# Optimization experiments

Measured on AMD Instinct MI355X. Metric: run time of the kernel, lower is better.

Reference implementation:

```python
import jax, jax.numpy as jnp
import numpy as np

BS = 32768
NIN = 512
E = 8          # num_experts
T = 2          # num_tasks
H = 256        # num_neurons_expert
NT = 1         # num_neurons_tower


def setup_inputs() -> dict:
    key = jax.random.key(0)
    ks = jax.random.split(key, 7)
    s_in = 1.0 / np.sqrt(NIN)
    s_h = 1.0 / np.sqrt(H)
    return {
        "xv": jax.random.normal(ks[0], (BS, NIN), dtype=jnp.float32),
        "We": jax.random.uniform(ks[1], (E, NIN, H), dtype=jnp.float32, minval=-s_in, maxval=s_in),
        "be": jax.random.uniform(ks[2], (E, H), dtype=jnp.float32, minval=-s_in, maxval=s_in),
        "Wg": jax.random.uniform(ks[3], (T, NIN, E), dtype=jnp.float32, minval=-s_in, maxval=s_in),
        "bg": jax.random.uniform(ks[4], (T, E), dtype=jnp.float32, minval=-s_in, maxval=s_in),
        "Wt": jax.random.uniform(ks[5], (T, H, NT), dtype=jnp.float32, minval=-s_h, maxval=s_h),
        "bt": jax.random.uniform(ks[6], (T, NT), dtype=jnp.float32, minval=-s_h, maxval=s_h),
        "bs": BS,
    }


def reference(xv, We, be, Wg, bg, Wt, bt, bs):
    # Experts: [bs, E, H] (dropout is identity in eval mode)
    out_experts = jax.nn.relu(jnp.einsum("bi,eih->beh", xv, We) + be[None, :, :])
    # Gates: [bs, T, E], softmax over experts
    gates = jax.nn.softmax(jnp.einsum("bi,tie->bte", xv, Wg) + bg[None, :, :], axis=-1)
    # Gated combine: [bs, T, H]
    input_towers = jnp.einsum("bte,beh->bth", gates, out_experts)
    # Towers: [bs, T, NT] -> squeeze NT=1 -> [bs, T]
    out_towers = jax.nn.relu(jnp.einsum("bth,thn->btn", input_towers, Wt) + bt[None, :, :])
    out = jax.nn.sigmoid(out_towers[:, :, 0])  # [bs, T]
    return (out[:, 0], out[:, 1])
```

## Files before the change

### kernel.cpp

```cpp
#include <hip/hip_runtime.h>

typedef __attribute__((ext_vector_type(8))) short short8;
typedef __attribute__((ext_vector_type(4))) float floatx4;
typedef __attribute__((ext_vector_type(4))) float f32x4;

#define BS   32768

__device__ __forceinline__ unsigned short f2bf(float f) {
  unsigned int u = __float_as_uint(f);
  u += 0x7fffu + ((u >> 16) & 1u);
  return (unsigned short)(u >> 16);
}

__global__ void prep_weT(const float* __restrict__ We, unsigned short* __restrict__ WeT) {
  int e  = blockIdx.x >> 6;
  int kc = blockIdx.x & 63;
  int h  = threadIdx.x;
  short8 pk;
#pragma unroll
  for (int j = 0; j < 8; ++j)
    pk[j] = (short)f2bf(We[e * 131072 + (kc * 8 + j) * 256 + h]);
  *reinterpret_cast<short8*>(&WeT[e * 131072 + h * 512 + kc * 8]) = pk;
}

__global__ void prep_wgT(const float* __restrict__ Wg, unsigned short* __restrict__ WgT) {
  int row = blockIdx.x;
  int t = row >> 3, e = row & 7;
  int lane = threadIdx.x;
  short8 pk;
#pragma unroll
  for (int j = 0; j < 8; ++j)
    pk[j] = (short)f2bf(Wg[t * 4096 + (lane * 8 + j) * 8 + e]);
  *reinterpret_cast<short8*>(&WgT[row * 512 + lane * 8]) = pk;
}

#define GLOAD16(SRC, DST) \
  __builtin_amdgcn_global_load_lds( \
      (const __attribute__((address_space(1))) unsigned int*)(SRC), \
      (__attribute__((address_space(3))) unsigned int*)(DST), 16, 0, 0)

__global__ __launch_bounds__(256) void conv_gates(
    const float* __restrict__ xv, const unsigned short* __restrict__ WgT,
    const float* __restrict__ bg, unsigned short* __restrict__ Abf,
    float* __restrict__ gates_ws)
{
  __shared__ __attribute__((aligned(16))) unsigned char bufA[65536];
  const int tid = threadIdx.x;
  const int b0  = blockIdx.x * 64;
  const int r8 = tid >> 3, kslot = tid & 7;
  const int mt = b0 >> 8;
  const int rc_base = b0 & 255;
  unsigned char* AbfB = reinterpret_cast<unsigned char*>(Abf);

#pragma unroll
  for (int pass = 0; pass < 2; ++pass) {
    int r = pass * 32 + r8;
    int r_c = rc_base + r;
    const float* xrow = xv + (size_t)(b0 + r) * 512;
    unsigned swz = (unsigned)((r & 7) << 4);
#pragma unroll
    for (int j = 0; j < 8; ++j) {
      int o = j * 8 + kslot;
      f32x4 v0 = *reinterpret_cast<const f32x4*>(xrow + o * 8);
      f32x4 v1 = *reinterpret_cast<const f32x4*>(xrow + o * 8 + 4);
      short8 pk;
      pk[0] = (short)f2bf(v0[0]); pk[1] = (short)f2bf(v0[1]);
      pk[2] = (short)f2bf(v0[2]); pk[3] = (short)f2bf(v0[3]);
      pk[4] = (short)f2bf(v1[0]); pk[5] = (short)f2bf(v1[1]);
      pk[6] = (short)f2bf(v1[2]); pk[7] = (short)f2bf(v1[3]);
      unsigned lb = ((unsigned)r << 10) + (((unsigned)(o * 16)) ^ swz);
      *reinterpret_cast<short8*>(&bufA[lb]) = pk;
      unsigned gb = (unsigned)((mt * 8 + j) * 32768) + (unsigned)(r_c * 128)
                  + (((unsigned)(kslot * 16)) ^ swz);
      *reinterpret_cast<short8*>(&AbfB[gb]) = pk;
    }
  }
  __syncthreads();

  const int wave = tid >> 6, lane = tid & 63;
  const int row16 = lane & 15, kgrp = lane >> 4;
  floatx4 gacc = {0.f, 0.f, 0.f, 0.f};
  const unsigned abase = ((unsigned)row16 << 10) + ((unsigned)kgrp << 4) + ((unsigned)wave << 14);
  const unsigned a_swz = (unsigned)((row16 & 7) << 4);
  const unsigned short* wg_lane = WgT + row16 * 512 + kgrp * 8;
#pragma unroll
  for (int ks = 0; ks < 16; ++ks) {
    short8 af = *reinterpret_cast<const short8*>(&bufA[(abase + (unsigned)(ks << 6)) ^ a_swz]);
    short8 bf = *reinterpret_cast<const short8*>(wg_lane + ks * 32);
    gacc = __builtin_amdgcn_mfma_f32_16x16x32_bf16(af, bf, gacc, 0, 0, 0);
  }
  float bgv = bg[row16];
#pragma unroll
  for (int j = 0; j < 4; ++j) {
    float v = gacc[j] + bgv;
    float mx = v;
    mx = fmaxf(mx, __shfl_xor(mx, 1));
    mx = fmaxf(mx, __shfl_xor(mx, 2));
    mx = fmaxf(mx, __shfl_xor(mx, 4));
    float p = __expf(v - mx);
    float s = p;
    s += __shfl_xor(s, 1);
    s += __shfl_xor(s, 2);
    s += __shfl_xor(s, 4);
    gates_ws[row16 * BS + b0 + wave * 16 + kgrp * 4 + j] = p / s;
  }
}

__global__ __launch_bounds__(512, 2) void mmoe_main(
    const unsigned short* __restrict__ Abf,
    const unsigned short* __restrict__ WeT,
    const float* __restrict__ gates_ws,
    const float* __restrict__ be,
    const float* __restrict__ Wt,
    float* __restrict__ acc_ws)
{
  __shared__ __attribute__((aligned(16))) unsigned char smem[131072];
  __shared__ float red_lds[4][256][2];

  const int tid = threadIdx.x, wave = tid >> 6, lane = tid & 63;
  const int row16 = lane & 15, kgrp = lane >> 4;
  const int wm = wave >> 2, wn = wave & 3;
  const int bid = blockIdx.x, e = bid & 7, mt = bid >> 3;

  const unsigned short* Asrc = Abf + (size_t)mt * 131072;
  const unsigned short* Bsrc = WeT + e * 131072;

  unsigned soffB[4];
#pragma unroll
  for (int i = 0; i < 4; ++i) {
    unsigned x = (unsigned)(i * 8192 + tid * 16);
    unsigned r = x >> 7;
    unsigned y = (x & 127u) ^ ((r & 7u) << 4);
    soffB[i] = r * 512u + (y >> 1);
  }
  const unsigned soffA0 = (unsigned)(tid * 8);

  unsigned char* Ab0 = smem;
  unsigned char* Ab1 = smem + 32768;
  unsigned char* Bb0 = smem + 65536;
  unsigned char* Bb1 = smem + 98304;

#pragma unroll
  for (int i = 0; i < 4; ++i)
    GLOAD16(Asrc + (i * 4096 + soffA0), Ab0 + (i * 8 + wave) * 1024);
#pragma unroll
  for (int i = 0; i < 4; ++i)
    GLOAD16(Bsrc + soffB[i], Bb0 + (i * 8 + wave) * 1024);

  floatx4 acc[8][4];
#pragma unroll
  for (int mf = 0; mf < 8; ++mf)
#pragma unroll
    for (int n = 0; n < 4; ++n) acc[mf][n] = (floatx4){0.f, 0.f, 0.f, 0.f};

  const unsigned swz = (unsigned)((row16 & 7) << 4);
  const unsigned bcol = (unsigned)(wn * 64 + row16);
  const unsigned arow = (unsigned)(wm * 128 + row16);

  for (int kc = 0; kc < 8; ++kc) {
    const int cur = kc & 1;
    if (kc < 7) {
      unsigned char* an = cur ? Ab0 : Ab1;
      unsigned char* bn = cur ? Bb0 : Bb1;
      const unsigned short* abase2 = Asrc + (kc + 1) * 16384;
      const unsigned short* bbase2 = Bsrc + (kc + 1) * 64;
#pragma unroll
      for (int i = 0; i < 4; ++i)
        GLOAD16(abase2 + (i * 4096 + soffA0), an + (i * 8 + wave) * 1024);
#pragma unroll
      for (int i = 0; i < 4; ++i)
        GLOAD16(bbase2 + soffB[i], bn + (i * 8 + wave) * 1024);
      asm volatile("s_waitcnt vmcnt(8)" ::: "memory");
    } else {
      asm volatile("s_waitcnt vmcnt(0)" ::: "memory");
    }
    __builtin_amdgcn_s_barrier();
    __builtin_amdgcn_sched_barrier(0);

    const unsigned char* ab = cur ? Ab1 : Ab0;
    const unsigned char* bb = cur ? Bb1 : Bb0;
    __builtin_amdgcn_s_setprio(1);
    short8 bf[2][4];
#pragma unroll
    for (int ks = 0; ks < 2; ++ks)
#pragma unroll
      for (int n = 0; n < 4; ++n)
        bf[ks][n] = *reinterpret_cast<const short8*>(
            &bb[(bcol + (unsigned)(n * 16)) * 128 + (((unsigned)(ks * 64 + kgrp * 16)) ^ swz)]);
#pragma unroll
    for (int mf = 0; mf < 8; ++mf) {
      const unsigned rb = (arow + (unsigned)(mf * 16)) * 128;
      short8 a0 = *reinterpret_cast<const short8*>(&ab[rb + (((unsigned)(kgrp * 16)) ^ swz)]);
      short8 a1 = *reinterpret_cast<const short8*>(&ab[rb + (((unsigned)(64 + kgrp * 16)) ^ swz)]);
#pragma unroll
      for (int n = 0; n < 4; ++n)
        acc[mf][n] = __builtin_amdgcn_mfma_f32_16x16x32_bf16(a0, bf[0][n], acc[mf][n], 0, 0, 0);
#pragma unroll
      for (int n = 0; n < 4; ++n)
        acc[mf][n] = __builtin_amdgcn_mfma_f32_16x16x32_bf16(a1, bf[1][n], acc[mf][n], 0, 0, 0);
    }
    __builtin_amdgcn_s_setprio(0);
    __builtin_amdgcn_s_barrier();
  }

  float bev[4], wtv[2][4];
#pragma unroll
  for (int n = 0; n < 4; ++n) bev[n] = be[e * 256 + wn * 64 + n * 16 + row16];
#pragma unroll
  for (int t = 0; t < 2; ++t)
#pragma unroll
    for (int n = 0; n < 4; ++n) wtv[t][n] = Wt[t * 256 + wn * 64 + n * 16 + row16];

#pragma unroll
  for (int mf = 0; mf < 8; ++mf) {
#pragma unroll
    for (int j = 0; j < 4; ++j) {
      float p0 = 0.f, p1 = 0.f;
#pragma unroll
      for (int n = 0; n < 4; ++n) {
        float r = fmaxf(acc[mf][n][j] + bev[n], 0.f);
        p0 = fmaf(r, wtv[0][n], p0);
        p1 = fmaf(r, wtv[1][n], p1);
      }
      p0 += __shfl_xor(p0, 1); p1 += __shfl_xor(p1, 1);
      p0 += __shfl_xor(p0, 2); p1 += __shfl_xor(p1, 2);
      p0 += __shfl_xor(p0, 4); p1 += __shfl_xor(p1, 4);
      p0 += __shfl_xor(p0, 8); p1 += __shfl_xor(p1, 8);
      if (row16 == 0) {
        int rw = wm * 128 + mf * 16 + kgrp * 4 + j;
        red_lds[wn][rw][0] = p0;
        red_lds[wn][rw][1] = p1;
      }
    }
  }
  __syncthreads();

  {
    int row = tid >> 1, t = tid & 1;
    float s = red_lds[0][row][t] + red_lds[1][row][t]
            + red_lds[2][row][t] + red_lds[3][row][t];
    float g = gates_ws[(t * 8 + e) * BS + mt * 256 + row];
    atomicAdd(&acc_ws[t * BS + mt * 256 + row], s * g);
  }
}

__global__ void finalize(const float* __restrict__ acc_ws, const float* __restrict__ bt,
                         float* __restrict__ out) {
  int i = blockIdx.x * 256 + threadIdx.x;
  int t = i >> 15;
  float s = fmaxf(acc_ws[i] + bt[t], 0.f);
  out[i] = 1.f / (1.f + __expf(-s));
}

extern "C" void kernel_launch(void* const* d_in, const int* in_sizes, int n_in,
                              void* d_out, int out_size, void* d_ws, size_t ws_size,
                              hipStream_t stream) {
  const float* xv = (const float*)d_in[0];
  const float* We = (const float*)d_in[1];
  const float* be = (const float*)d_in[2];
  const float* Wg = (const float*)d_in[3];
  const float* bg = (const float*)d_in[4];
  const float* Wt = (const float*)d_in[5];
  const float* bt = (const float*)d_in[6];
  float* out = (float*)d_out;

  unsigned char* ws = (unsigned char*)d_ws;
  unsigned short* WeT      = (unsigned short*)(ws);
  unsigned short* WgT      = (unsigned short*)(ws + (2u << 20));
  unsigned short* Abf      = (unsigned short*)(ws + (4u << 20));
  float*          gates_ws = (float*)(ws + (36u << 20));
  float*          acc_ws   = (float*)(ws + (38u << 20));

  hipMemsetAsync(acc_ws, 0, 2 * BS * sizeof(float), stream);
  prep_weT<<<512, 256, 0, stream>>>(We, WeT);
  prep_wgT<<<16, 64, 0, stream>>>(Wg, WgT);
  conv_gates<<<512, 256, 0, stream>>>(xv, WgT, bg, Abf, gates_ws);
  mmoe_main<<<1024, 512, 0, stream>>>(Abf, WeT, gates_ws, be, Wt, acc_ws);
  finalize<<<256, 256, 0, stream>>>(acc_ws, bt, out);
}
```

Before: 130.5 us.

## Split GEMM K-step into four phases interleaving prefetch with MFMA clusters

Restructures the double-buffered main loop into four phases per K tile. Each phase reads a pair of A fragments from LDS, issues part of the next tile's global-to-LDS loads, then runs a barrier-synchronised cluster of MFMAs at raised priority. The aim is to spread memory traffic across the compute and keep waves in lockstep, in the style of ping-pong scheduling. In exchange it adds many more barriers per iteration, and the prologue now waits for the whole first tile before starting.

```diff
diff --git a/kernel.cpp b/kernel.cpp
--- a/kernel.cpp
+++ b/kernel.cpp
@@ -146,6 +146,8 @@
 #pragma unroll
   for (int i = 0; i < 4; ++i)
     GLOAD16(Bsrc + soffB[i], Bb0 + (i * 8 + wave) * 1024);
+  asm volatile("s_waitcnt vmcnt(0)" ::: "memory");
+  __syncthreads();
 
   floatx4 acc[8][4];
 #pragma unroll
@@ -153,54 +155,134 @@
 #pragma unroll
     for (int n = 0; n < 4; ++n) acc[mf][n] = (floatx4){0.f, 0.f, 0.f, 0.f};
 
-  const unsigned swz = (unsigned)((row16 & 7) << 4);
+  const unsigned swz  = (unsigned)((row16 & 7) << 4);
   const unsigned bcol = (unsigned)(wn * 64 + row16);
   const unsigned arow = (unsigned)(wm * 128 + row16);
 
-  for (int kc = 0; kc < 8; ++kc) {
-    const int cur = kc & 1;
-    if (kc < 7) {
-      unsigned char* an = cur ? Ab0 : Ab1;
-      unsigned char* bn = cur ? Bb0 : Bb1;
-      const unsigned short* abase2 = Asrc + (kc + 1) * 16384;
-      const unsigned short* bbase2 = Bsrc + (kc + 1) * 64;
-#pragma unroll
-      for (int i = 0; i < 4; ++i)
-        GLOAD16(abase2 + (i * 4096 + soffA0), an + (i * 8 + wave) * 1024);
-#pragma unroll
-      for (int i = 0; i < 4; ++i)
-        GLOAD16(bbase2 + soffB[i], bn + (i * 8 + wave) * 1024);
-      asm volatile("s_waitcnt vmcnt(8)" ::: "memory");
-    } else {
-      asm volatile("s_waitcnt vmcnt(0)" ::: "memory");
-    }
-    __builtin_amdgcn_s_barrier();
+  for (int kt = 0; kt < 8; ++kt) {
     __builtin_amdgcn_sched_barrier(0);
-
+    const int cur = kt & 1;
     const unsigned char* ab = cur ? Ab1 : Ab0;
     const unsigned char* bb = cur ? Bb1 : Bb0;
-    __builtin_amdgcn_s_setprio(1);
+    unsigned char* an = cur ? Ab0 : Ab1;
+    unsigned char* bn = cur ? Bb0 : Bb1;
+    const unsigned short* aNext = Asrc + (kt + 1) * 16384;
+    const unsigned short* bNext = Bsrc + (kt + 1) * 64;
+
+    auto rdA = [&](int mf, int ks) -> short8 {
+      const unsigned rb = (arow + (unsigned)(mf * 16)) * 128;
+      return *reinterpret_cast<const short8*>(
+          &ab[rb + (((unsigned)(ks * 64 + kgrp * 16)) ^ swz)]);
+    };
+
     short8 bf[2][4];
-#pragma unroll
-    for (int ks = 0; ks < 2; ++ks)
-#pragma unroll
-      for (int n = 0; n < 4; ++n)
-        bf[ks][n] = *reinterpret_cast<const short8*>(
-            &bb[(bcol + (unsigned)(n * 16)) * 128 + (((unsigned)(ks * 64 + kgrp * 16)) ^ swz)]);
-#pragma unroll
-    for (int mf = 0; mf < 8; ++mf) {
-      const unsigned rb = (arow + (unsigned)(mf * 16)) * 128;
-      short8 a0 = *reinterpret_cast<const short8*>(&ab[rb + (((unsigned)(kgrp * 16)) ^ swz)]);
-      short8 a1 = *reinterpret_cast<const short8*>(&ab[rb + (((unsigned)(64 + kgrp * 16)) ^ swz)]);
-#pragma unroll
-      for (int n = 0; n < 4; ++n)
-        acc[mf][n] = __builtin_amdgcn_mfma_f32_16x16x32_bf16(a0, bf[0][n], acc[mf][n], 0, 0, 0);
-#pragma unroll
-      for (int n = 0; n < 4; ++n)
-        acc[mf][n] = __builtin_amdgcn_mfma_f32_16x16x32_bf16(a1, bf[1][n], acc[mf][n], 0, 0, 0);
-    }
-    __builtin_amdgcn_s_setprio(0);
-    __builtin_amdgcn_s_barrier();
+
+    {
+#pragma unroll
+      for (int ks = 0; ks < 2; ++ks)
+#pragma unroll
+        for (int n = 0; n < 4; ++n)
+          bf[ks][n] = *reinterpret_cast<const short8*>(
+              &bb[(bcol + (unsigned)(n * 16)) * 128 + (((unsigned)(ks * 64 + kgrp * 16)) ^ swz)]);
+      short8 p00 = rdA(0, 0), p01 = rdA(0, 1), p10 = rdA(1, 0), p11 = rdA(1, 1);
+      if (kt < 7) {
+#pragma unroll
+        for (int i = 0; i < 4; ++i)
+          GLOAD16(aNext + (i * 4096 + soffA0), an + (i * 8 + wave) * 1024);
+      }
+      asm volatile("s_waitcnt lgkmcnt(8)" ::: "memory");
+      __builtin_amdgcn_s_barrier();
+      asm volatile("s_waitcnt lgkmcnt(0)" ::: "memory");
+      __builtin_amdgcn_sched_barrier(0);
+      __builtin_amdgcn_s_setprio(1);
+#pragma unroll
+      for (int n = 0; n < 4; ++n)
+        acc[0][n] = __builtin_amdgcn_mfma_f32_16x16x32_bf16(p00, bf[0][n], acc[0][n], 0, 0, 0);
+#pragma unroll
+      for (int n = 0; n < 4; ++n)
+        acc[0][n] = __builtin_amdgcn_mfma_f32_16x16x32_bf16(p01, bf[1][n], acc[0][n], 0, 0, 0);
+#pragma unroll
+      for (int n = 0; n < 4; ++n)
+        acc[1][n] = __builtin_amdgcn_mfma_f32_16x16x32_bf16(p10, bf[0][n], acc[1][n], 0, 0, 0);
+#pragma unroll
+      for (int n = 0; n < 4; ++n)
+        acc[1][n] = __builtin_amdgcn_mfma_f32_16x16x32_bf16(p11, bf[1][n], acc[1][n], 0, 0, 0);
+      __builtin_amdgcn_s_setprio(0);
+      __builtin_amdgcn_s_barrier();
+    }
+
+    {
+      short8 p00 = rdA(2, 0), p01 = rdA(2, 1), p10 = rdA(3, 0), p11 = rdA(3, 1);
+      if (kt < 7) {
+#pragma unroll
+        for (int i = 0; i < 4; ++i)
+          GLOAD16(bNext + soffB[i], bn + (i * 8 + wave) * 1024);
+      }
+      __builtin_amdgcn_s_barrier();
+      asm volatile("s_waitcnt lgkmcnt(0)" ::: "memory");
+      __builtin_amdgcn_sched_barrier(0);
+      __builtin_amdgcn_s_setprio(1);
+#pragma unroll
+      for (int n = 0; n < 4; ++n)
+        acc[2][n] = __builtin_amdgcn_mfma_f32_16x16x32_bf16(p00, bf[0][n], acc[2][n], 0, 0, 0);
+#pragma unroll
+      for (int n = 0; n < 4; ++n)
+        acc[2][n] = __builtin_amdgcn_mfma_f32_16x16x32_bf16(p01, bf[1][n], acc[2][n], 0, 0, 0);
+#pragma unroll
+      for (int n = 0; n < 4; ++n)
+        acc[3][n] = __builtin_amdgcn_mfma_f32_16x16x32_bf16(p10, bf[0][n], acc[3][n], 0, 0, 0);
+#pragma unroll
+      for (int n = 0; n < 4; ++n)
+        acc[3][n] = __builtin_amdgcn_mfma_f32_16x16x32_bf16(p11, bf[1][n], acc[3][n], 0, 0, 0);
+      __builtin_amdgcn_s_setprio(0);
+      __builtin_amdgcn_s_barrier();
+    }
+
+    {
+      short8 p00 = rdA(4, 0), p01 = rdA(4, 1), p10 = rdA(5, 0), p11 = rdA(5, 1);
+      __builtin_amdgcn_s_barrier();
+      asm volatile("s_waitcnt lgkmcnt(0)" ::: "memory");
+      __builtin_amdgcn_sched_barrier(0);
+      __builtin_amdgcn_s_setprio(1);
+#pragma unroll
+      for (int n = 0; n < 4; ++n)
+        acc[4][n] = __builtin_amdgcn_mfma_f32_16x16x32_bf16(p00, bf[0][n], acc[4][n], 0, 0, 0);
+#pragma unroll
+      for (int n = 0; n < 4; ++n)
+        acc[4][n] = __builtin_amdgcn_mfma_f32_16x16x32_bf16(p01, bf[1][n], acc[4][n], 0, 0, 0);
+#pragma unroll
+      for (int n = 0; n < 4; ++n)
+        acc[5][n] = __builtin_amdgcn_mfma_f32_16x16x32_bf16(p10, bf[0][n], acc[5][n], 0, 0, 0);
+#pragma unroll
+      for (int n = 0; n < 4; ++n)
+        acc[5][n] = __builtin_amdgcn_mfma_f32_16x16x32_bf16(p11, bf[1][n], acc[5][n], 0, 0, 0);
+      __builtin_amdgcn_s_setprio(0);
+      __builtin_amdgcn_s_barrier();
+    }
+
+    {
+      short8 p00 = rdA(6, 0), p01 = rdA(6, 1), p10 = rdA(7, 0), p11 = rdA(7, 1);
+      if (kt < 7)
+        asm volatile("s_waitcnt vmcnt(0)" ::: "memory");
+      __builtin_amdgcn_s_barrier();
+      asm volatile("s_waitcnt lgkmcnt(0)" ::: "memory");
+      __builtin_amdgcn_sched_barrier(0);
+      __builtin_amdgcn_s_setprio(1);
+#pragma unroll
+      for (int n = 0; n < 4; ++n)
+        acc[6][n] = __builtin_amdgcn_mfma_f32_16x16x32_bf16(p00, bf[0][n], acc[6][n], 0, 0, 0);
+#pragma unroll
+      for (int n = 0; n < 4; ++n)
+        acc[6][n] = __builtin_amdgcn_mfma_f32_16x16x32_bf16(p01, bf[1][n], acc[6][n], 0, 0, 0);
+#pragma unroll
+      for (int n = 0; n < 4; ++n)
+        acc[7][n] = __builtin_amdgcn_mfma_f32_16x16x32_bf16(p10, bf[0][n], acc[7][n], 0, 0, 0);
+#pragma unroll
+      for (int n = 0; n < 4; ++n)
+        acc[7][n] = __builtin_amdgcn_mfma_f32_16x16x32_bf16(p11, bf[1][n], acc[7][n], 0, 0, 0);
+      __builtin_amdgcn_s_setprio(0);
+      __builtin_amdgcn_s_barrier();
+    }
   }
 
   float bev[4], wtv[2][4];
```

Result: faster. 124.9 us (-4.3%).

## Interleave LDS fragment reads with MFMA groups and stagger next-tile global loads

Applied to the files above, without the earlier changes.

The K-loop is fully unrolled, and the A-fragment LDS reads are split into four stages. Each stage's reads are issued before the previous stage's MFMA group, with lgkmcnt waits and sched_barriers, so LDS latency overlaps matrix math. The prefetch of the next tile is also split: A loads go out before the barrier and B loads go out mid-iteration, so the vmcnt wait only covers the older loads. This adds more registers for the in-flight fragments and relies on hand-placed counter waits, which could stall or raise register pressure if mistuned.

```diff
diff --git a/kernel.cpp b/kernel.cpp
--- a/kernel.cpp
+++ b/kernel.cpp
@@ -153,33 +153,39 @@
 #pragma unroll
     for (int n = 0; n < 4; ++n) acc[mf][n] = (floatx4){0.f, 0.f, 0.f, 0.f};
 
-  const unsigned swz = (unsigned)((row16 & 7) << 4);
+  const unsigned swz  = (unsigned)((row16 & 7) << 4);
   const unsigned bcol = (unsigned)(wn * 64 + row16);
   const unsigned arow = (unsigned)(wm * 128 + row16);
 
-  for (int kc = 0; kc < 8; ++kc) {
-    const int cur = kc & 1;
-    if (kc < 7) {
-      unsigned char* an = cur ? Ab0 : Ab1;
-      unsigned char* bn = cur ? Bb0 : Bb1;
-      const unsigned short* abase2 = Asrc + (kc + 1) * 16384;
-      const unsigned short* bbase2 = Bsrc + (kc + 1) * 64;
+#define RDA(AB, MF, KS) \
+  (*reinterpret_cast<const short8*>( \
+      &(AB)[(arow + (unsigned)((MF) * 16)) * 128 + (((unsigned)((KS) * 64 + kgrp * 16)) ^ swz)]))
+
+#define MFMA4(ACC, AV, BV) \
+  _Pragma("unroll") \
+  for (int n = 0; n < 4; ++n) \
+    ACC[n] = __builtin_amdgcn_mfma_f32_16x16x32_bf16(AV, BV[n], ACC[n], 0, 0, 0);
+
+#pragma unroll
+  for (int kt = 0; kt < 8; ++kt) {
+    const unsigned char* ab = (kt & 1) ? Ab1 : Ab0;
+    const unsigned char* bb = (kt & 1) ? Bb1 : Bb0;
+    unsigned char* an = (kt & 1) ? Ab0 : Ab1;
+    unsigned char* bn = (kt & 1) ? Bb0 : Bb1;
+    const unsigned short* aNext = Asrc + (kt + 1) * 16384;
+    const unsigned short* bNext = Bsrc + (kt + 1) * 64;
+
+    if (kt < 7) {
 #pragma unroll
       for (int i = 0; i < 4; ++i)
-        GLOAD16(abase2 + (i * 4096 + soffA0), an + (i * 8 + wave) * 1024);
-#pragma unroll
-      for (int i = 0; i < 4; ++i)
-        GLOAD16(bbase2 + soffB[i], bn + (i * 8 + wave) * 1024);
-      asm volatile("s_waitcnt vmcnt(8)" ::: "memory");
+        GLOAD16(aNext + (i * 4096 + soffA0), an + (i * 8 + wave) * 1024);
+      asm volatile("s_waitcnt vmcnt(4)" ::: "memory");
     } else {
       asm volatile("s_waitcnt vmcnt(0)" ::: "memory");
     }
     __builtin_amdgcn_s_barrier();
     __builtin_amdgcn_sched_barrier(0);
 
-    const unsigned char* ab = cur ? Ab1 : Ab0;
-    const unsigned char* bb = cur ? Bb1 : Bb0;
-    __builtin_amdgcn_s_setprio(1);
     short8 bf[2][4];
 #pragma unroll
     for (int ks = 0; ks < 2; ++ks)
@@ -187,21 +193,51 @@
       for (int n = 0; n < 4; ++n)
         bf[ks][n] = *reinterpret_cast<const short8*>(
             &bb[(bcol + (unsigned)(n * 16)) * 128 + (((unsigned)(ks * 64 + kgrp * 16)) ^ swz)]);
-#pragma unroll
-    for (int mf = 0; mf < 8; ++mf) {
-      const unsigned rb = (arow + (unsigned)(mf * 16)) * 128;
-      short8 a0 = *reinterpret_cast<const short8*>(&ab[rb + (((unsigned)(kgrp * 16)) ^ swz)]);
-      short8 a1 = *reinterpret_cast<const short8*>(&ab[rb + (((unsigned)(64 + kgrp * 16)) ^ swz)]);
-#pragma unroll
-      for (int n = 0; n < 4; ++n)
-        acc[mf][n] = __builtin_amdgcn_mfma_f32_16x16x32_bf16(a0, bf[0][n], acc[mf][n], 0, 0, 0);
-#pragma unroll
-      for (int n = 0; n < 4; ++n)
-        acc[mf][n] = __builtin_amdgcn_mfma_f32_16x16x32_bf16(a1, bf[1][n], acc[mf][n], 0, 0, 0);
+    short8 a00 = RDA(ab, 0, 0), a01 = RDA(ab, 0, 1);
+    short8 a10 = RDA(ab, 1, 0), a11 = RDA(ab, 1, 1);
+    short8 b00 = RDA(ab, 2, 0), b01 = RDA(ab, 2, 1);
+    short8 b10 = RDA(ab, 3, 0), b11 = RDA(ab, 3, 1);
+    asm volatile("s_waitcnt lgkmcnt(4)" ::: "memory");
+    __builtin_amdgcn_sched_barrier(0);
+    __builtin_amdgcn_s_setprio(1);
+    MFMA4(acc[0], a00, bf[0]); MFMA4(acc[0], a01, bf[1]);
+    MFMA4(acc[1], a10, bf[0]); MFMA4(acc[1], a11, bf[1]);
+    __builtin_amdgcn_s_setprio(0);
+
+    if (kt < 7) {
+#pragma unroll
+      for (int i = 0; i < 4; ++i)
+        GLOAD16(bNext + soffB[i], bn + (i * 8 + wave) * 1024);
     }
+    short8 c00 = RDA(ab, 4, 0), c01 = RDA(ab, 4, 1);
+    short8 c10 = RDA(ab, 5, 0), c11 = RDA(ab, 5, 1);
+    asm volatile("s_waitcnt lgkmcnt(4)" ::: "memory");
+    __builtin_amdgcn_sched_barrier(0);
+    __builtin_amdgcn_s_setprio(1);
+    MFMA4(acc[2], b00, bf[0]); MFMA4(acc[2], b01, bf[1]);
+    MFMA4(acc[3], b10, bf[0]); MFMA4(acc[3], b11, bf[1]);
+    __builtin_amdgcn_s_setprio(0);
+
+    short8 d00 = RDA(ab, 6, 0), d01 = RDA(ab, 6, 1);
+    short8 d10 = RDA(ab, 7, 0), d11 = RDA(ab, 7, 1);
+    asm volatile("s_waitcnt lgkmcnt(4)" ::: "memory");
+    __builtin_amdgcn_sched_barrier(0);
+    __builtin_amdgcn_s_setprio(1);
+    MFMA4(acc[4], c00, bf[0]); MFMA4(acc[4], c01, bf[1]);
+    MFMA4(acc[5], c10, bf[0]); MFMA4(acc[5], c11, bf[1]);
+    __builtin_amdgcn_s_setprio(0);
+
+    asm volatile("s_waitcnt lgkmcnt(0)" ::: "memory");
+    __builtin_amdgcn_sched_barrier(0);
+    __builtin_amdgcn_s_setprio(1);
+    MFMA4(acc[6], d00, bf[0]); MFMA4(acc[6], d01, bf[1]);
+    MFMA4(acc[7], d10, bf[0]); MFMA4(acc[7], d11, bf[1]);
     __builtin_amdgcn_s_setprio(0);
     __builtin_amdgcn_s_barrier();
-  }
+    __builtin_amdgcn_sched_barrier(0);
+  }
+#undef RDA
+#undef MFMA4
 
   float bev[4], wtv[2][4];
 #pragma unroll
```

Measured after the change: 127.6 us. 1.02x faster.
